# Kernel tuning notes

Hardware: AMD Instinct MI355X
Metric: run time of the kernel (lower is better)

## Reference

```python
import jax, jax.numpy as jnp
import numpy as np

LOG2 = float(np.log(2.0))

def _mlp(x, W, b):
    # SchNet-style MLP block: Linear + shifted softplus activation
    return jax.nn.softplus(x @ W + b) - LOG2

def setup_inputs() -> dict:
    key = jax.random.key(0)
    ks = jax.random.split(key, 9)
    E, N, R, F, O = 1_600_000, 50_000, 64, 64, 64
    s = 1.0 / np.sqrt(F)
    return {
        "bf": jax.random.normal(ks[0], (E, R), dtype=jnp.float32),
        "eh": jax.random.normal(ks[1], (E, F), dtype=jnp.float32),
        "W1": jax.random.normal(ks[2], (R, F), dtype=jnp.float32) * s,
        "b1": jax.random.normal(ks[3], (F,), dtype=jnp.float32) * s,
        "W2": jax.random.normal(ks[4], (F, F), dtype=jnp.float32) * s,
        "b2": jax.random.normal(ks[5], (F,), dtype=jnp.float32) * s,
        "W3": jax.random.normal(ks[6], (F, O), dtype=jnp.float32) * s,
        "b3": jax.random.normal(ks[7], (O,), dtype=jnp.float32) * s,
        "dst": jax.random.randint(ks[8], (E,), 0, N, dtype=jnp.int32),
        "num_nodes": N,
    }

def reference(bf, eh, W1, b1, W2, b2, W3, b3, dst, num_nodes):
    # Edge filter-generating network: two MLPs on radial basis features
    w = _mlp(_mlp(bf, W1, b1), W2, b2)          # [E, F]
    m = w * eh                                   # gated edge messages [E, F]
    # scatter-mean onto destination nodes (dgl copy_e + mean)
    sums = jax.ops.segment_sum(m, dst, num_segments=num_nodes)              # [N, F]
    cnt = jax.ops.segment_sum(jnp.ones((m.shape[0],), m.dtype), dst,
                              num_segments=num_nodes)                        # [N]
    h = sums / jnp.maximum(cnt, 1.0)[:, None]    # mean; 0 for isolated nodes
    return _mlp(h, W3, b3)                       # interaction-block MLP [N, O]
```

## Files before the change

kernel.cpp:

```cpp
#include <hip/hip_runtime.h>
#include <hip/hip_bf16.h>

#define LOG2F_ 0.69314718055994530942f

typedef __attribute__((ext_vector_type(8))) short s8bf;
typedef __attribute__((ext_vector_type(4))) float f32x4;
typedef __attribute__((ext_vector_type(4))) unsigned u32x4;

__device__ __forceinline__ float ssp(float x) {
    float e = __expf(-fabsf(x));
    return __logf(1.0f + e) + fmaxf(x, 0.0f) - LOG2F_;
}
__device__ __forceinline__ short bf_hi(float x) {
    __hip_bfloat16 h = __float2bfloat16(x);
    return *reinterpret_cast<short*>(&h);
}
__device__ __forceinline__ float bf_to_f(short s) {
    __hip_bfloat16 h;
    *reinterpret_cast<short*>(&h) = s;
    return __bfloat162float(h);
}
__device__ __forceinline__ unsigned pkhi(float a, float b) {
    return (__float_as_uint(a) >> 16) | (__float_as_uint(b) & 0xFFFF0000u);
}
__device__ __forceinline__ unsigned pklo(float a, float b) {
    float ra = a - __uint_as_float(__float_as_uint(a) & 0xFFFF0000u);
    float rb = b - __uint_as_float(__float_as_uint(b) & 0xFFFF0000u);
    return (__float_as_uint(ra) >> 16) | (__float_as_uint(rb) & 0xFFFF0000u);
}

__global__ __launch_bounds__(256) void hist_kernel(const int* __restrict__ dst,
                                                   int* __restrict__ hist, int E) {
    const int i0 = (blockIdx.x * blockDim.x + threadIdx.x) * 4;
    if (i0 + 3 < E) {
        int4 d = *(const int4*)(dst + i0);
        atomicAdd(&hist[d.x], 1); atomicAdd(&hist[d.y], 1);
        atomicAdd(&hist[d.z], 1); atomicAdd(&hist[d.w], 1);
    } else {
        for (int j = 0; j < 4; ++j)
            if (i0 + j < E) atomicAdd(&hist[dst[i0 + j]], 1);
    }
}

__global__ __launch_bounds__(256) void scan_part(const int* __restrict__ h,
                                                 int* __restrict__ bsum, int N) {
    const int i0 = blockIdx.x * 1024 + threadIdx.x * 4;
    int s = 0;
    #pragma unroll
    for (int j = 0; j < 4; ++j) { int i = i0 + j; if (i < N) s += h[i]; }
    __shared__ int red[4];
    const int lane = threadIdx.x & 63, w = threadIdx.x >> 6;
    #pragma unroll
    for (int off = 32; off; off >>= 1) s += __shfl_down(s, off, 64);
    if (lane == 0) red[w] = s;
    __syncthreads();
    if (threadIdx.x == 0) bsum[blockIdx.x] = red[0] + red[1] + red[2] + red[3];
}

__global__ void scan_top(int* __restrict__ bsum, int nb) {
    const int lane = threadIdx.x;
    if (nb <= 64) {
        int v = (lane < nb) ? bsum[lane] : 0;
        int inc = v;
        #pragma unroll
        for (int off = 1; off < 64; off <<= 1) {
            int o = __shfl_up(inc, off, 64);
            if (lane >= off) inc += o;
        }
        if (lane < nb) bsum[lane] = inc - v;
    } else if (lane == 0) {
        int run = 0;
        for (int i = 0; i < nb; ++i) { int t = bsum[i]; bsum[i] = run; run += t; }
    }
}

__global__ __launch_bounds__(256) void scan_local(const int* __restrict__ h,
                                                  const int* __restrict__ bsum,
                                                  int* __restrict__ cursor, int N) {
    const int i0 = blockIdx.x * 1024 + threadIdx.x * 4;
    int v[4]; int s = 0;
    #pragma unroll
    for (int j = 0; j < 4; ++j) { int i = i0 + j; v[j] = (i < N) ? h[i] : 0; s += v[j]; }
    const int lane = threadIdx.x & 63, w = threadIdx.x >> 6;
    int inc = s;
    #pragma unroll
    for (int off = 1; off < 64; off <<= 1) {
        int o = __shfl_up(inc, off, 64);
        if (lane >= off) inc += o;
    }
    __shared__ int wsum[4];
    if (lane == 63) wsum[w] = inc;
    __syncthreads();
    int run = bsum[blockIdx.x];
    for (int i = 0; i < w; ++i) run += wsum[i];
    run += inc - s;
    #pragma unroll
    for (int j = 0; j < 4; ++j) { int i = i0 + j; if (i < N) cursor[i] = run; run += v[j]; }
}

__global__ __launch_bounds__(256) void rank_kernel(const int* __restrict__ dst,
                                                   int* __restrict__ cursor,
                                                   int2* __restrict__ meta, int E) {
    const int i0 = (blockIdx.x * blockDim.x + threadIdx.x) * 4;
    if (i0 + 3 < E) {
        int4 d = *(const int4*)(dst + i0);
        int p0 = atomicAdd(&cursor[d.x], 1); meta[p0] = make_int2(i0,     d.x);
        int p1 = atomicAdd(&cursor[d.y], 1); meta[p1] = make_int2(i0 + 1, d.y);
        int p2 = atomicAdd(&cursor[d.z], 1); meta[p2] = make_int2(i0 + 2, d.z);
        int p3 = atomicAdd(&cursor[d.w], 1); meta[p3] = make_int2(i0 + 3, d.w);
    } else {
        for (int j = 0; j < 4; ++j)
            if (i0 + j < E) {
                int dd = dst[i0 + j];
                int p = atomicAdd(&cursor[dd], 1);
                meta[p] = make_int2(i0 + j, dd);
            }
    }
}

#define WFRAG(woff, nt, k0i) \
    (*(const s8bf*)(lds + (woff) + ((((nt) << 1) + (k0i)) << 10) + (lane << 4)))

__global__ __launch_bounds__(256, 3) void edge_kernel(
    const float* __restrict__ bf, const float* __restrict__ eh,
    const float* __restrict__ W1, const float* __restrict__ b1,
    const float* __restrict__ W2, const float* __restrict__ b2,
    const int2* __restrict__ meta,
    float* __restrict__ sums, int E)
{
    __shared__ __align__(16) unsigned char lds[49152];

    const int tid  = threadIdx.x;
    const int lane = tid & 63;
    const int wv   = tid >> 6;
    const int g    = lane >> 4;
    const int n16  = lane & 15;

    {
        float* wst = (float*)(lds + 32768);
        for (int i = tid; i < 4096; i += 256) wst[i] = W1[i];
        __syncthreads();
        for (int u = tid; u < 512; u += 256) {
            const int f = u >> 6, nt = f >> 1, k0i = f & 1;
            const int gg = (u >> 4) & 3, nn = u & 15;
            s8bf hi, lo;
            #pragma unroll
            for (int j = 0; j < 8; ++j) {
                float v = wst[(k0i * 32 + gg * 8 + j) * 64 + nt * 16 + nn];
                short h = bf_hi(v);
                hi[j] = h; lo[j] = bf_hi(v - bf_to_f(h));
            }
            *(s8bf*)(lds + (u << 4)) = hi;
            *(s8bf*)(lds + 8192 + (u << 4)) = lo;
        }
        __syncthreads();
        for (int i = tid; i < 4096; i += 256) wst[i] = W2[i];
        __syncthreads();
        for (int u = tid; u < 512; u += 256) {
            const int f = u >> 6, nt = f >> 1, k0i = f & 1;
            const int gg = (u >> 4) & 3, nn = u & 15;
            s8bf hi, lo;
            #pragma unroll
            for (int j = 0; j < 8; ++j) {
                float v = wst[(k0i * 32 + gg * 8 + j) * 64 + nt * 16 + nn];
                short h = bf_hi(v);
                hi[j] = h; lo[j] = bf_hi(v - bf_to_f(h));
            }
            *(s8bf*)(lds + 16384 + (u << 4)) = hi;
            *(s8bf*)(lds + 24576 + (u << 4)) = lo;
        }
        __syncthreads();
    }

    float b1v[4], b2v[4];
    #pragma unroll
    for (int nt = 0; nt < 4; ++nt) { b1v[nt] = b1[nt*16 + n16]; b2v[nt] = b2[nt*16 + n16]; }

    unsigned char* wb = lds + 32768 + (wv << 12);
    char* Xh = (char*)wb;
    char* Xl = (char*)wb + 2048;

    const int r4   = lane >> 2;
    const int c16  = (lane & 3) << 4;
    const int s0   = (lane & 3) << 1;
    const int crow = g << 2;
    const int sw_n = (n16 & 7) << 4;

    const int wave_id = (blockIdx.x << 2) + wv;
    const int nwaves  = gridDim.x << 2;
    const int ntiles  = (E + 15) >> 4;
    const int lastE   = E - 1;

    int eiv0 = 0, eiv1 = 0, dsv0 = 0, dsv1 = 0;
    float xs[16];
    {
        const int t1 = wave_id + nwaves;
        if (lane < 16) {
            if (wave_id < ntiles) {
                const int2 mv = meta[min(wave_id * 16 + lane, lastE)];
                eiv0 = mv.x; dsv0 = mv.y;
            }
            if (t1 < ntiles) {
                const int2 mv = meta[min(t1 * 16 + lane, lastE)];
                eiv1 = mv.x; dsv1 = mv.y;
            }
        }
        if (wave_id < ntiles) {
            const int ri = __shfl(eiv0, r4, 64);
            const size_t roff = (size_t)(unsigned)ri * 64 + c16;
            *(float4*)&xs[0]  = *(const float4*)(bf + roff);
            *(float4*)&xs[4]  = *(const float4*)(bf + roff + 4);
            *(float4*)&xs[8]  = *(const float4*)(bf + roff + 8);
            *(float4*)&xs[12] = *(const float4*)(bf + roff + 12);
        }
    }

    for (int t = wave_id; t < ntiles; t += nwaves) {
        const int base = t << 4;

        u32x4 hv0, hv1, lv0, lv1;
        #pragma unroll
        for (int j = 0; j < 4; ++j) {
            hv0[j] = pkhi(xs[2*j],     xs[2*j + 1]);
            lv0[j] = pklo(xs[2*j],     xs[2*j + 1]);
            hv1[j] = pkhi(xs[8 + 2*j], xs[8 + 2*j + 1]);
            lv1[j] = pklo(xs[8 + 2*j], xs[8 + 2*j + 1]);
        }
        {
            const int sw = (r4 & 7) << 4;
            const int a0 = r4 * 128 + ((s0 << 4) ^ sw);
            const int a1 = r4 * 128 + (((s0 + 1) << 4) ^ sw);
            *(u32x4*)(Xh + a0) = hv0;  *(u32x4*)(Xh + a1) = hv1;
            *(u32x4*)(Xl + a0) = lv0;  *(u32x4*)(Xl + a1) = lv1;
        }

        float evs[16];
        #pragma unroll
        for (int e = 0; e < 16; ++e) {
            const int ei = __builtin_amdgcn_readlane(eiv0, e);
            evs[e] = eh[(size_t)(unsigned)ei * 64 + lane];
        }

        const int tn1 = t + nwaves, tn2 = t + 2 * nwaves;
        if (tn1 < ntiles) {
            const int ri = __shfl(eiv1, r4, 64);
            const size_t roff = (size_t)(unsigned)ri * 64 + c16;
            *(float4*)&xs[0]  = *(const float4*)(bf + roff);
            *(float4*)&xs[4]  = *(const float4*)(bf + roff + 4);
            *(float4*)&xs[8]  = *(const float4*)(bf + roff + 8);
            *(float4*)&xs[12] = *(const float4*)(bf + roff + 12);
        }

        int eiv_n = 0, dsv_n = 0;
        if (lane < 16 && tn2 < ntiles) {
            const int2 mv = meta[min(tn2 * 16 + lane, lastE)];
            eiv_n = mv.x; dsv_n = mv.y;
        }

        f32x4 acc[4];
        #pragma unroll
        for (int nt = 0; nt < 4; ++nt) acc[nt] = (f32x4){0.f, 0.f, 0.f, 0.f};
        #pragma unroll
        for (int k0i = 0; k0i < 2; ++k0i) {
            const int ab = (n16 << 7) + (((((k0i << 2) + g)) << 4) ^ sw_n);
            s8bf ah = *(s8bf*)(Xh + ab);
            s8bf al = *(s8bf*)(Xl + ab);
            s8bf wh0 = WFRAG(0, 0, k0i), wh1 = WFRAG(0, 1, k0i),
                 wh2 = WFRAG(0, 2, k0i), wh3 = WFRAG(0, 3, k0i);
            s8bf wl0 = WFRAG(8192, 0, k0i), wl1 = WFRAG(8192, 1, k0i),
                 wl2 = WFRAG(8192, 2, k0i), wl3 = WFRAG(8192, 3, k0i);
            __builtin_amdgcn_s_setprio(1);
            acc[0] = __builtin_amdgcn_mfma_f32_16x16x32_bf16(ah, wh0, acc[0], 0, 0, 0);
            acc[0] = __builtin_amdgcn_mfma_f32_16x16x32_bf16(ah, wl0, acc[0], 0, 0, 0);
            acc[0] = __builtin_amdgcn_mfma_f32_16x16x32_bf16(al, wh0, acc[0], 0, 0, 0);
            acc[1] = __builtin_amdgcn_mfma_f32_16x16x32_bf16(ah, wh1, acc[1], 0, 0, 0);
            acc[1] = __builtin_amdgcn_mfma_f32_16x16x32_bf16(ah, wl1, acc[1], 0, 0, 0);
            acc[1] = __builtin_amdgcn_mfma_f32_16x16x32_bf16(al, wh1, acc[1], 0, 0, 0);
            acc[2] = __builtin_amdgcn_mfma_f32_16x16x32_bf16(ah, wh2, acc[2], 0, 0, 0);
            acc[2] = __builtin_amdgcn_mfma_f32_16x16x32_bf16(ah, wl2, acc[2], 0, 0, 0);
            acc[2] = __builtin_amdgcn_mfma_f32_16x16x32_bf16(al, wh2, acc[2], 0, 0, 0);
            acc[3] = __builtin_amdgcn_mfma_f32_16x16x32_bf16(ah, wh3, acc[3], 0, 0, 0);
            acc[3] = __builtin_amdgcn_mfma_f32_16x16x32_bf16(ah, wl3, acc[3], 0, 0, 0);
            acc[3] = __builtin_amdgcn_mfma_f32_16x16x32_bf16(al, wh3, acc[3], 0, 0, 0);
            __builtin_amdgcn_s_setprio(0);
        }

        #pragma unroll
        for (int nt = 0; nt < 4; ++nt)
            #pragma unroll
            for (int r = 0; r < 4; ++r) {
                const int row = crow + r;
                *(float*)(wb + (row << 8) +
                          ((((nt * 16 + n16) << 2)) ^ ((row & 7) << 4))) =
                    ssp(acc[nt][r] + b1v[nt]);
            }

        f32x4 acc2[4];
        #pragma unroll
        for (int nt = 0; nt < 4; ++nt) acc2[nt] = (f32x4){0.f, 0.f, 0.f, 0.f};
        #pragma unroll
        for (int k0i = 0; k0i < 2; ++k0i) {
            const int bc = (k0i << 7) + (g << 5);
            const int rb = n16 << 8;
            f32x4 f0 = *(f32x4*)(wb + rb + (bc ^ sw_n));
            f32x4 f1 = *(f32x4*)(wb + rb + ((bc + 16) ^ sw_n));
            u32x4 ahu, alu;
            ahu[0] = pkhi(f0[0], f0[1]); ahu[1] = pkhi(f0[2], f0[3]);
            ahu[2] = pkhi(f1[0], f1[1]); ahu[3] = pkhi(f1[2], f1[3]);
            alu[0] = pklo(f0[0], f0[1]); alu[1] = pklo(f0[2], f0[3]);
            alu[2] = pklo(f1[0], f1[1]); alu[3] = pklo(f1[2], f1[3]);
            s8bf ah = *(s8bf*)&ahu;
            s8bf al = *(s8bf*)&alu;
            s8bf wh0 = WFRAG(16384, 0, k0i), wh1 = WFRAG(16384, 1, k0i),
                 wh2 = WFRAG(16384, 2, k0i), wh3 = WFRAG(16384, 3, k0i);
            s8bf wl0 = WFRAG(24576, 0, k0i), wl1 = WFRAG(24576, 1, k0i),
                 wl2 = WFRAG(24576, 2, k0i), wl3 = WFRAG(24576, 3, k0i);
            __builtin_amdgcn_s_setprio(1);
            acc2[0] = __builtin_amdgcn_mfma_f32_16x16x32_bf16(ah, wh0, acc2[0], 0, 0, 0);
            acc2[0] = __builtin_amdgcn_mfma_f32_16x16x32_bf16(ah, wl0, acc2[0], 0, 0, 0);
            acc2[0] = __builtin_amdgcn_mfma_f32_16x16x32_bf16(al, wh0, acc2[0], 0, 0, 0);
            acc2[1] = __builtin_amdgcn_mfma_f32_16x16x32_bf16(ah, wh1, acc2[1], 0, 0, 0);
            acc2[1] = __builtin_amdgcn_mfma_f32_16x16x32_bf16(ah, wl1, acc2[1], 0, 0, 0);
            acc2[1] = __builtin_amdgcn_mfma_f32_16x16x32_bf16(al, wh1, acc2[1], 0, 0, 0);
            acc2[2] = __builtin_amdgcn_mfma_f32_16x16x32_bf16(ah, wh2, acc2[2], 0, 0, 0);
            acc2[2] = __builtin_amdgcn_mfma_f32_16x16x32_bf16(ah, wl2, acc2[2], 0, 0, 0);
            acc2[2] = __builtin_amdgcn_mfma_f32_16x16x32_bf16(al, wh2, acc2[2], 0, 0, 0);
            acc2[3] = __builtin_amdgcn_mfma_f32_16x16x32_bf16(ah, wh3, acc2[3], 0, 0, 0);
            acc2[3] = __builtin_amdgcn_mfma_f32_16x16x32_bf16(ah, wl3, acc2[3], 0, 0, 0);
            acc2[3] = __builtin_amdgcn_mfma_f32_16x16x32_bf16(al, wh3, acc2[3], 0, 0, 0);
            __builtin_amdgcn_s_setprio(0);
        }

        #pragma unroll
        for (int nt = 0; nt < 4; ++nt)
            #pragma unroll
            for (int r = 0; r < 4; ++r) {
                const int row = crow + r;
                *(float*)(wb + (row << 8) +
                          ((((nt * 16 + n16) << 2)) ^ ((row & 7) << 4))) =
                    ssp(acc2[nt][r] + b2v[nt]);
            }

        {
            float accv = 0.f;
            int cur = -1;
            #pragma unroll
            for (int e = 0; e < 16; ++e) {
                if (base + e < E) {
                    const int d = __builtin_amdgcn_readlane(dsv0, e);
                    const float mv = *(const float*)(wb + (e << 8) +
                                        ((lane << 2) ^ ((e & 7) << 4))) * evs[e];
                    if (d != cur) {
                        if (cur >= 0) atomicAdd(&sums[(size_t)cur * 64 + lane], accv);
                        accv = mv; cur = d;
                    } else {
                        accv += mv;
                    }
                }
            }
            if (cur >= 0) atomicAdd(&sums[(size_t)cur * 64 + lane], accv);
        }

        eiv0 = eiv1; eiv1 = eiv_n;
        dsv0 = dsv1; dsv1 = dsv_n;
    }
}

__global__ __launch_bounds__(256) void node_kernel(
    const float* __restrict__ sums, const int* __restrict__ hist,
    const float* __restrict__ W3, const float* __restrict__ b3,
    float* __restrict__ out, int N)
{
    __shared__ float sW[64][64];
    __shared__ float sb[64];
    __shared__ float sC[64];
    __shared__ float sX[64][65];

    const int tid = threadIdx.x;
    for (int i = tid; i < 4096; i += 256) sW[i >> 6][i & 63] = W3[i];
    if (tid < 64) sb[tid] = b3[tid];

    const int f4 = (tid & 15) << 2;
    const int e4 = (tid >> 4) << 2;
    const int ntiles = (N + 63) >> 6;

    for (int t = blockIdx.x; t < ntiles; t += gridDim.x) {
        const int base = t << 6;
        __syncthreads();
        if (tid < 64) {
            int gn = base + tid;
            sC[tid] = (gn < N) ? 1.0f / fmaxf((float)hist[gn], 1.0f) : 0.0f;
        }
        __syncthreads();
        #pragma unroll
        for (int k = 0; k < 16; ++k) {
            int idx = (k << 8) + tid;
            int n = idx >> 6, r = idx & 63;
            int gn = base + n;
            sX[n][r] = (gn < N) ? sums[(size_t)gn * 64 + r] * sC[n] : 0.0f;
        }
        __syncthreads();

        float acc[4][4] = {{0.f,0.f,0.f,0.f},{0.f,0.f,0.f,0.f},
                           {0.f,0.f,0.f,0.f},{0.f,0.f,0.f,0.f}};
        #pragma unroll 8
        for (int r = 0; r < 64; ++r) {
            float xv[4];
            #pragma unroll
            for (int i = 0; i < 4; ++i) xv[i] = sX[e4 + i][r];
            float4 w4 = *(const float4*)&sW[r][f4];
            #pragma unroll
            for (int i = 0; i < 4; ++i) {
                acc[i][0] = fmaf(xv[i], w4.x, acc[i][0]);
                acc[i][1] = fmaf(xv[i], w4.y, acc[i][1]);
                acc[i][2] = fmaf(xv[i], w4.z, acc[i][2]);
                acc[i][3] = fmaf(xv[i], w4.w, acc[i][3]);
            }
        }

        #pragma unroll
        for (int i = 0; i < 4; ++i) {
            int gn = base + e4 + i;
            if (gn < N) {
                float4 o;
                o.x = ssp(acc[i][0] + sb[f4 + 0]);
                o.y = ssp(acc[i][1] + sb[f4 + 1]);
                o.z = ssp(acc[i][2] + sb[f4 + 2]);
                o.w = ssp(acc[i][3] + sb[f4 + 3]);
                *(float4*)&out[(size_t)gn * 64 + f4] = o;
            }
        }
    }
}

extern "C" void kernel_launch(void* const* d_in, const int* in_sizes, int n_in,
                              void* d_out, int out_size, void* d_ws, size_t ws_size,
                              hipStream_t stream) {
    const float* bf = (const float*)d_in[0];
    const float* eh = (const float*)d_in[1];
    const float* W1 = (const float*)d_in[2];
    const float* b1 = (const float*)d_in[3];
    const float* W2 = (const float*)d_in[4];
    const float* b2 = (const float*)d_in[5];
    const float* W3 = (const float*)d_in[6];
    const float* b3 = (const float*)d_in[7];
    const int*   dst = (const int*)d_in[8];

    const int E = in_sizes[0] / 64;
    const int N = out_size / 64;

    float* sums    = (float*)d_ws;
    int*   hist    = (int*)(sums + (size_t)N * 64);
    int*   cursor  = hist + N;
    int2*  meta    = (int2*)(cursor + N);
    int*   bsum    = (int*)(meta + E);

    hipMemsetAsync(d_ws, 0, (size_t)N * 64 * sizeof(float) + N * sizeof(int), stream);

    const int gE4 = (E + 1023) / 1024;
    const int nb  = (N + 1023) >> 10;
    hist_kernel<<<gE4, 256, 0, stream>>>(dst, hist, E);
    scan_part<<<nb, 256, 0, stream>>>(hist, bsum, N);
    scan_top<<<1, 64, 0, stream>>>(bsum, nb);
    scan_local<<<nb, 256, 0, stream>>>(hist, bsum, cursor, N);
    rank_kernel<<<gE4, 256, 0, stream>>>(dst, cursor, meta, E);

    edge_kernel<<<2048, 256, 0, stream>>>(bf, eh, W1, b1, W2, b2, meta, sums, E);

    const int ntilesN = (N + 63) >> 6;
    node_kernel<<<ntilesN, 256, 0, stream>>>(sums, hist, W3, b3, (float*)d_out, N);
}
```

Measured before the change: 467.4 us.

## Move low-part weight fragments to global memory to shrink LDS and raise occupancy

A small pre-kernel now computes the bf16 low-residual weight fragments for W1 and W2 and writes them to workspace. The edge kernel keeps only the high parts in LDS and reads the low parts straight from global memory (served by cache), cutting LDS per block from 48KB to 32KB. This allows launch bounds of 4 blocks per CU instead of 3, with the grid halved to 1024 blocks. The cost is extra global/cache loads of weight fragments in the inner MFMA loop and one more kernel launch.

```diff
diff --git a/kernel.cpp b/kernel.cpp
--- a/kernel.cpp
+++ b/kernel.cpp
@@ -118,17 +118,39 @@
     }
 }
 
+__global__ __launch_bounds__(256) void wsplit_kernel(
+    const float* __restrict__ W1, const float* __restrict__ W2,
+    unsigned char* __restrict__ wlg)
+{
+    const float* W = blockIdx.x ? W2 : W1;
+    unsigned char* out = wlg + blockIdx.x * 8192;
+    for (int u = threadIdx.x; u < 512; u += 256) {
+        const int f = u >> 6, nt = f >> 1, k0i = f & 1;
+        const int gg = (u >> 4) & 3, nn = u & 15;
+        s8bf lo;
+        #pragma unroll
+        for (int j = 0; j < 8; ++j) {
+            float v = W[(k0i * 32 + gg * 8 + j) * 64 + nt * 16 + nn];
+            short h = bf_hi(v);
+            lo[j] = bf_hi(v - bf_to_f(h));
+        }
+        *(s8bf*)(out + (u << 4)) = lo;
+    }
+}
+
 #define WFRAG(woff, nt, k0i) \
     (*(const s8bf*)(lds + (woff) + ((((nt) << 1) + (k0i)) << 10) + (lane << 4)))
-
-__global__ __launch_bounds__(256, 3) void edge_kernel(
+#define WFRAGG(moff, nt, k0i) \
+    (*(const s8bf*)(wlg + (moff) + ((((nt) << 1) + (k0i)) << 10) + (lane << 4)))
+
+__global__ __launch_bounds__(256, 4) void edge_kernel(
     const float* __restrict__ bf, const float* __restrict__ eh,
     const float* __restrict__ W1, const float* __restrict__ b1,
     const float* __restrict__ W2, const float* __restrict__ b2,
-    const int2* __restrict__ meta,
+    const int2* __restrict__ meta, const unsigned char* __restrict__ wlg,
     float* __restrict__ sums, int E)
 {
-    __shared__ __align__(16) unsigned char lds[49152];
+    __shared__ __align__(16) unsigned char lds[32768];
 
     const int tid  = threadIdx.x;
     const int lane = tid & 63;
@@ -137,21 +159,17 @@
     const int n16  = lane & 15;
 
     {
-        float* wst = (float*)(lds + 32768);
+        float* wst = (float*)(lds + 16384);
         for (int i = tid; i < 4096; i += 256) wst[i] = W1[i];
         __syncthreads();
         for (int u = tid; u < 512; u += 256) {
             const int f = u >> 6, nt = f >> 1, k0i = f & 1;
             const int gg = (u >> 4) & 3, nn = u & 15;
-            s8bf hi, lo;
-            #pragma unroll
-            for (int j = 0; j < 8; ++j) {
-                float v = wst[(k0i * 32 + gg * 8 + j) * 64 + nt * 16 + nn];
-                short h = bf_hi(v);
-                hi[j] = h; lo[j] = bf_hi(v - bf_to_f(h));
-            }
+            s8bf hi;
+            #pragma unroll
+            for (int j = 0; j < 8; ++j)
+                hi[j] = bf_hi(wst[(k0i * 32 + gg * 8 + j) * 64 + nt * 16 + nn]);
             *(s8bf*)(lds + (u << 4)) = hi;
-            *(s8bf*)(lds + 8192 + (u << 4)) = lo;
         }
         __syncthreads();
         for (int i = tid; i < 4096; i += 256) wst[i] = W2[i];
@@ -159,15 +177,11 @@
         for (int u = tid; u < 512; u += 256) {
             const int f = u >> 6, nt = f >> 1, k0i = f & 1;
             const int gg = (u >> 4) & 3, nn = u & 15;
-            s8bf hi, lo;
-            #pragma unroll
-            for (int j = 0; j < 8; ++j) {
-                float v = wst[(k0i * 32 + gg * 8 + j) * 64 + nt * 16 + nn];
-                short h = bf_hi(v);
-                hi[j] = h; lo[j] = bf_hi(v - bf_to_f(h));
-            }
-            *(s8bf*)(lds + 16384 + (u << 4)) = hi;
-            *(s8bf*)(lds + 24576 + (u << 4)) = lo;
+            s8bf hi;
+            #pragma unroll
+            for (int j = 0; j < 8; ++j)
+                hi[j] = bf_hi(wst[(k0i * 32 + gg * 8 + j) * 64 + nt * 16 + nn]);
+            *(s8bf*)(lds + 8192 + (u << 4)) = hi;
         }
         __syncthreads();
     }
@@ -176,7 +190,7 @@
     #pragma unroll
     for (int nt = 0; nt < 4; ++nt) { b1v[nt] = b1[nt*16 + n16]; b2v[nt] = b2[nt*16 + n16]; }
 
-    unsigned char* wb = lds + 32768 + (wv << 12);
+    unsigned char* wb = lds + 16384 + (wv << 12);
     char* Xh = (char*)wb;
     char* Xl = (char*)wb + 2048;
 
@@ -263,12 +277,12 @@
         #pragma unroll
         for (int k0i = 0; k0i < 2; ++k0i) {
             const int ab = (n16 << 7) + (((((k0i << 2) + g)) << 4) ^ sw_n);
+            s8bf wl0 = WFRAGG(0, 0, k0i), wl1 = WFRAGG(0, 1, k0i),
+                 wl2 = WFRAGG(0, 2, k0i), wl3 = WFRAGG(0, 3, k0i);
             s8bf ah = *(s8bf*)(Xh + ab);
             s8bf al = *(s8bf*)(Xl + ab);
             s8bf wh0 = WFRAG(0, 0, k0i), wh1 = WFRAG(0, 1, k0i),
                  wh2 = WFRAG(0, 2, k0i), wh3 = WFRAG(0, 3, k0i);
-            s8bf wl0 = WFRAG(8192, 0, k0i), wl1 = WFRAG(8192, 1, k0i),
-                 wl2 = WFRAG(8192, 2, k0i), wl3 = WFRAG(8192, 3, k0i);
             __builtin_amdgcn_s_setprio(1);
             acc[0] = __builtin_amdgcn_mfma_f32_16x16x32_bf16(ah, wh0, acc[0], 0, 0, 0);
             acc[0] = __builtin_amdgcn_mfma_f32_16x16x32_bf16(ah, wl0, acc[0], 0, 0, 0);
@@ -302,6 +316,8 @@
         for (int k0i = 0; k0i < 2; ++k0i) {
             const int bc = (k0i << 7) + (g << 5);
             const int rb = n16 << 8;
+            s8bf wl0 = WFRAGG(8192, 0, k0i), wl1 = WFRAGG(8192, 1, k0i),
+                 wl2 = WFRAGG(8192, 2, k0i), wl3 = WFRAGG(8192, 3, k0i);
             f32x4 f0 = *(f32x4*)(wb + rb + (bc ^ sw_n));
             f32x4 f1 = *(f32x4*)(wb + rb + ((bc + 16) ^ sw_n));
             u32x4 ahu, alu;
@@ -311,10 +327,8 @@
             alu[2] = pklo(f1[0], f1[1]); alu[3] = pklo(f1[2], f1[3]);
             s8bf ah = *(s8bf*)&ahu;
             s8bf al = *(s8bf*)&alu;
-            s8bf wh0 = WFRAG(16384, 0, k0i), wh1 = WFRAG(16384, 1, k0i),
-                 wh2 = WFRAG(16384, 2, k0i), wh3 = WFRAG(16384, 3, k0i);
-            s8bf wl0 = WFRAG(24576, 0, k0i), wl1 = WFRAG(24576, 1, k0i),
-                 wl2 = WFRAG(24576, 2, k0i), wl3 = WFRAG(24576, 3, k0i);
+            s8bf wh0 = WFRAG(8192, 0, k0i), wh1 = WFRAG(8192, 1, k0i),
+                 wh2 = WFRAG(8192, 2, k0i), wh3 = WFRAG(8192, 3, k0i);
             __builtin_amdgcn_s_setprio(1);
             acc2[0] = __builtin_amdgcn_mfma_f32_16x16x32_bf16(ah, wh0, acc2[0], 0, 0, 0);
             acc2[0] = __builtin_amdgcn_mfma_f32_16x16x32_bf16(ah, wl0, acc2[0], 0, 0, 0);
@@ -449,23 +463,25 @@
     const int E = in_sizes[0] / 64;
     const int N = out_size / 64;
 
-    float* sums    = (float*)d_ws;
+    unsigned char* wlg = (unsigned char*)d_ws;
+    float* sums    = (float*)(wlg + 16384);
     int*   hist    = (int*)(sums + (size_t)N * 64);
     int*   cursor  = hist + N;
     int2*  meta    = (int2*)(cursor + N);
     int*   bsum    = (int*)(meta + E);
 
-    hipMemsetAsync(d_ws, 0, (size_t)N * 64 * sizeof(float) + N * sizeof(int), stream);
+    hipMemsetAsync(sums, 0, (size_t)N * 64 * sizeof(float) + N * sizeof(int), stream);
 
     const int gE4 = (E + 1023) / 1024;
     const int nb  = (N + 1023) >> 10;
+    wsplit_kernel<<<2, 256, 0, stream>>>(W1, W2, wlg);
     hist_kernel<<<gE4, 256, 0, stream>>>(dst, hist, E);
     scan_part<<<nb, 256, 0, stream>>>(hist, bsum, N);
     scan_top<<<1, 64, 0, stream>>>(bsum, nb);
     scan_local<<<nb, 256, 0, stream>>>(hist, bsum, cursor, N);
     rank_kernel<<<gE4, 256, 0, stream>>>(dst, cursor, meta, E);
 
-    edge_kernel<<<2048, 256, 0, stream>>>(bf, eh, W1, b1, W2, b2, meta, sums, E);
+    edge_kernel<<<1024, 256, 0, stream>>>(bf, eh, W1, b1, W2, b2, meta, wlg, sums, E);
 
     const int ntilesN = (N + 63) >> 6;
     node_kernel<<<ntilesN, 256, 0, stream>>>(sums, hist, W3, b3, (float*)d_out, N);
```

Measured after the change: 705.4 us. 1.51x slower.
